# Kernel optimization log

Measured on AMD Instinct MI355X. Metric: run time of the kernel, lower is better.

The kernel has to match this reference:

```python
import jax, jax.numpy as jnp
import numpy as np

MAX_NODE = 20
SEG = [100, 20, 3200, 160, 400, 20, 400]  # split sizes, total 4300

_DIMS = {"h1": (5, 16), "h2": (16, 8), "h3": (8, 8),
         "f1": (8, 16), "f2": (16, 8), "f3": (8, 8),
         "d1": (13, 16), "d2": (16, 8), "d3": (8, 8),
         "g1": (8, 16), "g2": (16, 8), "g3": (8, 8),
         "fc1": (29, 32), "fc2": (32, 16), "fc3": (16, 8), "fc4": (8, 1)}


def _mk(key, shape):
    return jax.random.normal(key, shape, dtype=jnp.float32) * 0.1


def setup_inputs() -> dict:
    key = jax.random.key(0)
    ks = jax.random.split(key, 8 + 2 * len(_DIMS))
    # assemble the flat [1,4300] input: node feats, masks/adjacency summaries
    ni = jax.random.normal(ks[0], (100,), dtype=jnp.float32)
    valid = jax.random.bernoulli(ks[1], 0.8, (20,)).astype(jnp.float32)
    gmats = jax.random.uniform(ks[2], (3200,), dtype=jnp.float32)
    gmasks = jax.random.bernoulli(ks[3], 0.5, (160,)).astype(jnp.float32)
    summ = jax.random.bernoulli(ks[4], 0.3, (400,)).astype(jnp.float32)
    running = jax.random.bernoulli(ks[5], 0.5, (20,)).astype(jnp.float32)
    backmap = jax.random.bernoulli(ks[6], 0.3, (400,)).astype(jnp.float32)
    inp = jnp.concatenate([ni, valid, gmats, gmasks, summ, running, backmap])[None, :]
    out = {"input": inp}
    i = 8
    for name, (din, dout) in _DIMS.items():
        out[name + "_w"] = _mk(ks[i], (din, dout)); i += 1
        out[name + "_b"] = _mk(ks[i], (dout,)); i += 1
    return out


def reference(input, h1_w, h1_b, h2_w, h2_b, h3_w, h3_b,
              f1_w, f1_b, f2_w, f2_b, f3_w, f3_b,
              d1_w, d1_b, d2_w, d2_b, d3_w, d3_b,
              g1_w, g1_b, g2_w, g2_b, g3_w, g3_b,
              fc1_w, fc1_b, fc2_w, fc2_b, fc3_w, fc3_b, fc4_w, fc4_b):
    relu = jax.nn.relu
    gl = lambda x, w, b: x @ w + b
    x0 = input[0]
    ni = x0[:100].reshape(MAX_NODE, 5)
    valid = x0[100:120].reshape(1, 1, MAX_NODE)
    # x0[120:3320] = gcn_mats (split in original but never used)
    summ = x0[3480:3880].reshape(1, MAX_NODE, MAX_NODE)
    running = x0[3880:3900].reshape(1, 1, MAX_NODE)
    backmap = x0[3900:4300].reshape(1, MAX_NODE, MAX_NODE)
    # original overwrites every gcn_mask with zeros(20,1)
    zmask = jnp.zeros((MAX_NODE, 1), dtype=input.dtype)

    def fblock(y):
        for w, b in ((f1_w, f1_b), (f2_w, f2_b), (f3_w, f3_b),
                     (f1_w, f1_b), (f2_w, f2_b), (f3_w, f3_b)):
            y = relu(gl(y, w, b))
        return y

    x = relu(gl(ni, h1_w, h1_b))
    x = relu(gl(x, h2_w, h2_b))
    x = relu(gl(x, h3_w, h3_b))  # (20, 8)
    y = x
    for blk in range(8):
        src = y if blk == 5 else x  # block 5 forgets to reset y = x (as in source)
        y = fblock(src) * zmask
        x = x + y
    gcn_output = x  # (20, 8)

    xc = jnp.concatenate([ni, gcn_output], axis=1)  # (20, 13)
    s = relu(gl(xc, d1_w, d1_b))
    s = relu(gl(s, d2_w, d2_b))
    s = relu(gl(s, d3_w, d3_b))
    s = jnp.matmul(summ, s)  # (1, 20, 8)
    dag_summary = s
    s = relu(gl(s, g1_w, g1_b))
    s = relu(gl(s, g2_w, g2_b))
    s = relu(gl(s, g3_w, g3_b))
    global_summary = jnp.matmul(running, s)  # (1, 1, 8)
    dag_ext = jnp.matmul(backmap, dag_summary)  # (1, 20, 8)
    glob_ext = jnp.tile(global_summary, (1, MAX_NODE, 1))  # (1, 20, 8)

    merge = jnp.concatenate([ni[None], gcn_output[None], dag_ext, glob_ext], axis=2)  # (1,20,29)
    y2 = relu(gl(merge, fc1_w, fc1_b))
    y2 = relu(gl(y2, fc2_w, fc2_b))
    y2 = relu(gl(y2, fc3_w, fc3_b))
    logits = gl(y2, fc4_w, fc4_b).reshape(1, 1, MAX_NODE)
    logits = logits + (valid - 1.0) * 10000.0
    return jax.nn.softmax(logits, axis=-1).reshape(1, MAX_NODE)
```

## Files before the change

### kernel.cpp

```cpp
#include <hip/hip_runtime.h>
#include <math.h>

#define NT 64

#define CP4(dst, src, n) do { \
    const float4* _s4 = (const float4*)(src); float4* _d4 = (float4*)(dst); \
    for (int i = tid; i < (n) / 4; i += NT) _d4[i] = _s4[i]; } while (0)

template<int DIN, int DOUT, bool RELU>
__device__ __forceinline__ void dense20(int tid, const float* __restrict__ in,
                                        const float* __restrict__ w,
                                        const float* __restrict__ bi,
                                        float* __restrict__ out) {
    constexpr int N = 20 * DOUT;
    #pragma unroll
    for (int i0 = 0; i0 < N; i0 += NT) {
        int i = i0 + tid;
        if (i < N) {
            int r = i / DOUT, c = i % DOUT;
            float acc = bi[c];
            #pragma unroll
            for (int k = 0; k < DIN; ++k)
                acc = fmaf(in[r * DIN + k], w[k * DOUT + c], acc);
            out[i] = RELU ? fmaxf(acc, 0.0f) : acc;
        }
    }
}

__global__ __launch_bounds__(NT)
void fused_net_kernel(const float* __restrict__ inp,
                      const float* __restrict__ h1w, const float* __restrict__ h1b,
                      const float* __restrict__ h2w, const float* __restrict__ h2b,
                      const float* __restrict__ h3w, const float* __restrict__ h3b,
                      const float* __restrict__ d1w, const float* __restrict__ d1b,
                      const float* __restrict__ d2w, const float* __restrict__ d2b,
                      const float* __restrict__ d3w, const float* __restrict__ d3b,
                      const float* __restrict__ g1w, const float* __restrict__ g1b,
                      const float* __restrict__ g2w, const float* __restrict__ g2b,
                      const float* __restrict__ g3w, const float* __restrict__ g3b,
                      const float* __restrict__ fc1w, const float* __restrict__ fc1b,
                      const float* __restrict__ fc2w, const float* __restrict__ fc2b,
                      const float* __restrict__ fc3w, const float* __restrict__ fc3b,
                      const float* __restrict__ fc4w, const float* __restrict__ fc4b,
                      float* __restrict__ out) {
    const int tid = threadIdx.x;

    __shared__ __align__(16) float s_ni[100];
    __shared__ __align__(16) float s_valid[20];
    __shared__ __align__(16) float s_summ[400];
    __shared__ __align__(16) float s_run[20];
    __shared__ __align__(16) float s_back[400];
    __shared__ __align__(16) float s_h1w[80],  s_h1b[16];
    __shared__ __align__(16) float s_h2w[128], s_h2b[8];
    __shared__ __align__(16) float s_h3w[64],  s_h3b[8];
    __shared__ __align__(16) float s_d1w[208], s_d1b[16];
    __shared__ __align__(16) float s_d2w[128], s_d2b[8];
    __shared__ __align__(16) float s_d3w[64],  s_d3b[8];
    __shared__ __align__(16) float s_g1w[128], s_g1b[16];
    __shared__ __align__(16) float s_g2w[128], s_g2b[8];
    __shared__ __align__(16) float s_g3w[64],  s_g3b[8];
    __shared__ __align__(16) float s_fc1w[928], s_fc1b[32];
    __shared__ __align__(16) float s_fc2w[512], s_fc2b[16];
    __shared__ __align__(16) float s_fc3w[128], s_fc3b[8];
    __shared__ __align__(16) float s_fc4w[8];
    __shared__ float s_fc4b[1];
    __shared__ __align__(16) float s_bufA[640];
    __shared__ __align__(16) float s_bufB[640];
    __shared__ __align__(16) float s_gcn[160];
    __shared__ __align__(16) float s_dag[160];
    __shared__ __align__(16) float s_glob[8];
    __shared__ __align__(16) float s_logit[20];

    CP4(s_ni,    inp,        100);
    CP4(s_valid, inp + 100,  20);
    CP4(s_summ,  inp + 3480, 400);
    CP4(s_run,   inp + 3880, 20);
    CP4(s_back,  inp + 3900, 400);
    CP4(s_h1w, h1w, 80);   CP4(s_h1b, h1b, 16);
    CP4(s_h2w, h2w, 128);  CP4(s_h2b, h2b, 8);
    CP4(s_h3w, h3w, 64);   CP4(s_h3b, h3b, 8);
    CP4(s_d1w, d1w, 208);  CP4(s_d1b, d1b, 16);
    CP4(s_d2w, d2w, 128);  CP4(s_d2b, d2b, 8);
    CP4(s_d3w, d3w, 64);   CP4(s_d3b, d3b, 8);
    CP4(s_g1w, g1w, 128);  CP4(s_g1b, g1b, 16);
    CP4(s_g2w, g2w, 128);  CP4(s_g2b, g2b, 8);
    CP4(s_g3w, g3w, 64);   CP4(s_g3b, g3b, 8);
    CP4(s_fc1w, fc1w, 928); CP4(s_fc1b, fc1b, 32);
    CP4(s_fc2w, fc2w, 512); CP4(s_fc2b, fc2b, 16);
    CP4(s_fc3w, fc3w, 128); CP4(s_fc3b, fc3b, 8);
    CP4(s_fc4w, fc4w, 8);
    if (tid == 0) s_fc4b[0] = fc4b[0];
    __syncthreads();

    dense20<5, 16, true>(tid, s_ni,   s_h1w, s_h1b, s_bufA); __syncthreads();
    dense20<16, 8, true>(tid, s_bufA, s_h2w, s_h2b, s_bufB); __syncthreads();
    dense20<8,  8, true>(tid, s_bufB, s_h3w, s_h3b, s_gcn);  __syncthreads();

    #pragma unroll
    for (int i0 = 0; i0 < 320; i0 += NT) {
        int i = i0 + tid;
        int r = i >> 4, c = i & 15;
        float acc = s_d1b[c];
        #pragma unroll
        for (int k = 0; k < 5; ++k)
            acc = fmaf(s_ni[r * 5 + k], s_d1w[k * 16 + c], acc);
        #pragma unroll
        for (int k = 0; k < 8; ++k)
            acc = fmaf(s_gcn[r * 8 + k], s_d1w[(5 + k) * 16 + c], acc);
        s_bufA[i] = fmaxf(acc, 0.0f);
    }
    __syncthreads();
    dense20<16, 8, true>(tid, s_bufA, s_d2w, s_d2b, s_bufB); __syncthreads();
    dense20<8,  8, true>(tid, s_bufB, s_d3w, s_d3b, s_bufA); __syncthreads();

    #pragma unroll
    for (int i0 = 0; i0 < 192; i0 += NT) {
        int i = i0 + tid;
        if (i < 160) {
            int r = i >> 3, c = i & 7;
            float acc = 0.0f;
            #pragma unroll
            for (int k = 0; k < 20; ++k)
                acc = fmaf(s_summ[r * 20 + k], s_bufA[k * 8 + c], acc);
            s_dag[i] = acc;
        }
    }
    __syncthreads();

    dense20<8, 16, true>(tid, s_dag,  s_g1w, s_g1b, s_bufA); __syncthreads();
    dense20<16, 8, true>(tid, s_bufA, s_g2w, s_g2b, s_bufB); __syncthreads();
    dense20<8,  8, true>(tid, s_bufB, s_g3w, s_g3b, s_bufA); __syncthreads();

    #pragma unroll
    for (int i0 = 0; i0 < 192; i0 += NT) {
        int i = i0 + tid;
        if (i < 160) {
            int r = i >> 3, c = i & 7;
            float acc = 0.0f;
            #pragma unroll
            for (int k = 0; k < 20; ++k)
                acc = fmaf(s_back[r * 20 + k], s_dag[k * 8 + c], acc);
            s_bufB[i] = acc;
        } else if (i < 168) {
            int c = i - 160;
            float acc = 0.0f;
            #pragma unroll
            for (int k = 0; k < 20; ++k)
                acc = fmaf(s_run[k], s_bufA[k * 8 + c], acc);
            s_glob[c] = acc;
        }
    }
    __syncthreads();

    #pragma unroll
    for (int i0 = 0; i0 < 640; i0 += NT) {
        int i = i0 + tid;
        int r = i >> 5, c = i & 31;
        float acc = s_fc1b[c];
        #pragma unroll
        for (int k = 0; k < 5; ++k)
            acc = fmaf(s_ni[r * 5 + k], s_fc1w[k * 32 + c], acc);
        #pragma unroll
        for (int k = 0; k < 8; ++k)
            acc = fmaf(s_gcn[r * 8 + k], s_fc1w[(5 + k) * 32 + c], acc);
        #pragma unroll
        for (int k = 0; k < 8; ++k)
            acc = fmaf(s_bufB[r * 8 + k], s_fc1w[(13 + k) * 32 + c], acc);
        #pragma unroll
        for (int k = 0; k < 8; ++k)
            acc = fmaf(s_glob[k], s_fc1w[(21 + k) * 32 + c], acc);
        s_bufA[i] = fmaxf(acc, 0.0f);
    }
    __syncthreads();
    dense20<32, 16, true>(tid, s_bufA, s_fc2w, s_fc2b, s_bufB); __syncthreads();
    dense20<16, 8, true>(tid, s_bufB, s_fc3w, s_fc3b, s_dag);   __syncthreads();

    if (tid < 20) {
        float acc = s_fc4b[0];
        #pragma unroll
        for (int k = 0; k < 8; ++k)
            acc = fmaf(s_dag[tid * 8 + k], s_fc4w[k], acc);
        s_logit[tid] = acc + (s_valid[tid] - 1.0f) * 10000.0f;
    }
    __syncthreads();

    if (tid < 20) {
        float m = s_logit[0];
        #pragma unroll
        for (int r = 1; r < 20; ++r) m = fmaxf(m, s_logit[r]);
        float sum = 0.0f;
        #pragma unroll
        for (int r = 0; r < 20; ++r) sum += __expf(s_logit[r] - m);
        out[tid] = __expf(s_logit[tid] - m) / sum;
    }
}

extern "C" void kernel_launch(void* const* d_in, const int* in_sizes, int n_in,
                              void* d_out, int out_size, void* d_ws, size_t ws_size,
                              hipStream_t stream) {
    const float* inp = (const float*)d_in[0];
    const float* h1w = (const float*)d_in[1];  const float* h1b = (const float*)d_in[2];
    const float* h2w = (const float*)d_in[3];  const float* h2b = (const float*)d_in[4];
    const float* h3w = (const float*)d_in[5];  const float* h3b = (const float*)d_in[6];
    const float* d1w = (const float*)d_in[13]; const float* d1b = (const float*)d_in[14];
    const float* d2w = (const float*)d_in[15]; const float* d2b = (const float*)d_in[16];
    const float* d3w = (const float*)d_in[17]; const float* d3b = (const float*)d_in[18];
    const float* g1w = (const float*)d_in[19]; const float* g1b = (const float*)d_in[20];
    const float* g2w = (const float*)d_in[21]; const float* g2b = (const float*)d_in[22];
    const float* g3w = (const float*)d_in[23]; const float* g3b = (const float*)d_in[24];
    const float* fc1w = (const float*)d_in[25]; const float* fc1b = (const float*)d_in[26];
    const float* fc2w = (const float*)d_in[27]; const float* fc2b = (const float*)d_in[28];
    const float* fc3w = (const float*)d_in[29]; const float* fc3b = (const float*)d_in[30];
    const float* fc4w = (const float*)d_in[31]; const float* fc4b = (const float*)d_in[32];
    float* out = (float*)d_out;

    fused_net_kernel<<<1, NT, 0, stream>>>(inp,
        h1w, h1b, h2w, h2b, h3w, h3b,
        d1w, d1b, d2w, d2b, d3w, d3b,
        g1w, g1b, g2w, g2b, g3w, g3b,
        fc1w, fc1b, fc2w, fc2b, fc3w, fc3b, fc4w, fc4b,
        out);
}
```

Before: 130.1 us.

## Replace unrolled per-layer code with table-driven layer interpreter in shared arena

Rewrites the fused MLP kernel as a generic loop over a constant-memory layer descriptor table, with all weights and activations in one shared arena and concatenated inputs materialized explicitly. Block size grows from 64 to 256 threads and helper functions are noinline with unrolling disabled to shrink code size. The intent is to cut instruction footprint (icache misses) and spread work across more threads, at the cost of runtime-indexed loops, constant-memory descriptor loads and less compile-time specialization.

```diff
diff --git a/kernel.cpp b/kernel.cpp
--- a/kernel.cpp
+++ b/kernel.cpp
@@ -1,30 +1,87 @@
 #include <hip/hip_runtime.h>
 #include <math.h>
 
-#define NT 64
+#define NT 256
 
-#define CP4(dst, src, n) do { \
-    const float4* _s4 = (const float4*)(src); float4* _d4 = (float4*)(dst); \
-    for (int i = tid; i < (n) / 4; i += NT) _d4[i] = _s4[i]; } while (0)
+enum : int {
+  O_ZERO = 0,
+  O_NI   = 32,
+  O_VALID= 132,
+  O_SUMM = 152,
+  O_RUN  = 552,
+  O_BACK = 572,
+  O_H1W  = 972,    O_H1B = 1052,
+  O_H2W  = 1068,   O_H2B = 1196,
+  O_H3W  = 1204,   O_H3B = 1268,
+  O_D1W  = 1276,   O_D1B = 1484,
+  O_D2W  = 1500,   O_D2B = 1628,
+  O_D3W  = 1636,   O_D3B = 1700,
+  O_G1W  = 1708,   O_G1B = 1836,
+  O_G2W  = 1852,   O_G2B = 1980,
+  O_G3W  = 1988,   O_G3B = 2052,
+  O_FC1W = 2060,   O_FC1B = 2988,
+  O_FC2W = 3020,   O_FC2B = 3532,
+  O_FC3W = 3548,   O_FC3B = 3676,
+  O_FC4W = 3684,   O_FC4B = 3692,
+  O_B0   = 3696,
+  O_B1   = 4336,
+  O_GCN  = 4656,
+  O_CC1  = 4816,
+  O_CC2  = 5076,
+  O_DAG  = 5656,
+  O_DAGX = 5816,
+  O_GLOB = 5976,
+  O_LOGIT= 5984,
+  ARENA  = 6004
+};
 
-template<int DIN, int DOUT, bool RELU>
-__device__ __forceinline__ void dense20(int tid, const float* __restrict__ in,
-                                        const float* __restrict__ w,
-                                        const float* __restrict__ bi,
-                                        float* __restrict__ out) {
-    constexpr int N = 20 * DOUT;
-    #pragma unroll
-    for (int i0 = 0; i0 < N; i0 += NT) {
-        int i = i0 + tid;
-        if (i < N) {
-            int r = i / DOUT, c = i % DOUT;
-            float acc = bi[c];
-            #pragma unroll
-            for (int k = 0; k < DIN; ++k)
-                acc = fmaf(in[r * DIN + k], w[k * DOUT + c], acc);
-            out[i] = RELU ? fmaxf(acc, 0.0f) : acc;
-        }
+struct Ld { int rows, din, p, in, w, b, out, relu; };
+
+__constant__ Ld LT[16] = {
+  {20,  5, 4, O_NI,   O_H1W,  O_H1B,  O_B0,   1},
+  {20, 16, 3, O_B0,   O_H2W,  O_H2B,  O_B1,   1},
+  {20,  8, 3, O_B1,   O_H3W,  O_H3B,  O_GCN,  1},
+  {20, 13, 4, O_CC1,  O_D1W,  O_D1B,  O_B0,   1},
+  {20, 16, 3, O_B0,   O_D2W,  O_D2B,  O_B1,   1},
+  {20,  8, 3, O_B1,   O_D3W,  O_D3B,  O_B0,   1},
+  {20, 20, 3, O_SUMM, O_B0,   O_ZERO, O_DAG,  0},
+  {20,  8, 4, O_DAG,  O_G1W,  O_G1B,  O_B0,   1},
+  {20, 16, 3, O_B0,   O_G2W,  O_G2B,  O_B1,   1},
+  {20,  8, 3, O_B1,   O_G3W,  O_G3B,  O_B0,   1},
+  {20, 20, 3, O_BACK, O_DAG,  O_ZERO, O_DAGX, 0},
+  { 1, 20, 3, O_RUN,  O_B0,   O_ZERO, O_GLOB, 0},
+  {20, 29, 5, O_CC2,  O_FC1W, O_FC1B, O_B0,   1},
+  {20, 32, 4, O_B0,   O_FC2W, O_FC2B, O_B1,   1},
+  {20, 16, 3, O_B1,   O_FC3W, O_FC3B, O_B0,   1},
+  {20,  8, 0, O_B0,   O_FC4W, O_FC4B, O_LOGIT,0},
+};
+
+__device__ __attribute__((noinline))
+void run_layers(float* A, int lo, int hi, int tid) {
+  #pragma clang loop unroll(disable)
+  for (int L = lo; L < hi; ++L) {
+    Ld d = LT[L];
+    const int N = d.rows << d.p, msk = (1 << d.p) - 1, st = 1 << d.p;
+    #pragma clang loop unroll(disable)
+    for (int i = tid; i < N; i += NT) {
+      const int r = i >> d.p, c = i & msk;
+      float acc = A[d.b + c];
+      const float* in = A + d.in + r * d.din;
+      const float* wp = A + d.w + c;
+      #pragma unroll 4
+      for (int k = 0; k < d.din; ++k) { acc = fmaf(in[k], *wp, acc); wp += st; }
+      A[d.out + i] = d.relu ? fmaxf(acc, 0.0f) : acc;
     }
+    __syncthreads();
+  }
+}
+
+__device__ __attribute__((noinline))
+void cp4(float* A, int dst, const float* __restrict__ src, int n, int tid) {
+  float4* d4 = (float4*)(A + dst);
+  const float4* s4 = (const float4*)src;
+  #pragma clang loop unroll(disable)
+  for (int i = tid; i < (n >> 2); i += NT) d4[i] = s4[i];
 }
 
 __global__ __launch_bounds__(NT)
@@ -43,181 +100,99 @@
                       const float* __restrict__ fc3w, const float* __restrict__ fc3b,
                       const float* __restrict__ fc4w, const float* __restrict__ fc4b,
                       float* __restrict__ out) {
-    const int tid = threadIdx.x;
+  const int tid = threadIdx.x;
+  __shared__ __align__(16) float A[ARENA];
 
-    __shared__ __align__(16) float s_ni[100];
-    __shared__ __align__(16) float s_valid[20];
-    __shared__ __align__(16) float s_summ[400];
-    __shared__ __align__(16) float s_run[20];
-    __shared__ __align__(16) float s_back[400];
-    __shared__ __align__(16) float s_h1w[80],  s_h1b[16];
-    __shared__ __align__(16) float s_h2w[128], s_h2b[8];
-    __shared__ __align__(16) float s_h3w[64],  s_h3b[8];
-    __shared__ __align__(16) float s_d1w[208], s_d1b[16];
-    __shared__ __align__(16) float s_d2w[128], s_d2b[8];
-    __shared__ __align__(16) float s_d3w[64],  s_d3b[8];
-    __shared__ __align__(16) float s_g1w[128], s_g1b[16];
-    __shared__ __align__(16) float s_g2w[128], s_g2b[8];
-    __shared__ __align__(16) float s_g3w[64],  s_g3b[8];
-    __shared__ __align__(16) float s_fc1w[928], s_fc1b[32];
-    __shared__ __align__(16) float s_fc2w[512], s_fc2b[16];
-    __shared__ __align__(16) float s_fc3w[128], s_fc3b[8];
-    __shared__ __align__(16) float s_fc4w[8];
-    __shared__ float s_fc4b[1];
-    __shared__ __align__(16) float s_bufA[640];
-    __shared__ __align__(16) float s_bufB[640];
-    __shared__ __align__(16) float s_gcn[160];
-    __shared__ __align__(16) float s_dag[160];
-    __shared__ __align__(16) float s_glob[8];
-    __shared__ __align__(16) float s_logit[20];
+  if (tid < 32) A[O_ZERO + tid] = 0.0f;
+  cp4(A, O_NI,    inp,        100, tid);
+  cp4(A, O_VALID, inp + 100,  20,  tid);
+  cp4(A, O_SUMM,  inp + 3480, 400, tid);
+  cp4(A, O_RUN,   inp + 3880, 20,  tid);
+  cp4(A, O_BACK,  inp + 3900, 400, tid);
+  cp4(A, O_H1W, h1w, 80, tid);   cp4(A, O_H1B, h1b, 16, tid);
+  cp4(A, O_H2W, h2w, 128, tid);  cp4(A, O_H2B, h2b, 8, tid);
+  cp4(A, O_H3W, h3w, 64, tid);   cp4(A, O_H3B, h3b, 8, tid);
+  cp4(A, O_D1W, d1w, 208, tid);  cp4(A, O_D1B, d1b, 16, tid);
+  cp4(A, O_D2W, d2w, 128, tid);  cp4(A, O_D2B, d2b, 8, tid);
+  cp4(A, O_D3W, d3w, 64, tid);   cp4(A, O_D3B, d3b, 8, tid);
+  cp4(A, O_G1W, g1w, 128, tid);  cp4(A, O_G1B, g1b, 16, tid);
+  cp4(A, O_G2W, g2w, 128, tid);  cp4(A, O_G2B, g2b, 8, tid);
+  cp4(A, O_G3W, g3w, 64, tid);   cp4(A, O_G3B, g3b, 8, tid);
+  cp4(A, O_FC1W, fc1w, 928, tid); cp4(A, O_FC1B, fc1b, 32, tid);
+  cp4(A, O_FC2W, fc2w, 512, tid); cp4(A, O_FC2B, fc2b, 16, tid);
+  cp4(A, O_FC3W, fc3w, 128, tid); cp4(A, O_FC3B, fc3b, 8, tid);
+  cp4(A, O_FC4W, fc4w, 8, tid);
+  if (tid == 0) A[O_FC4B] = fc4b[0];
+  __syncthreads();
 
-    CP4(s_ni,    inp,        100);
-    CP4(s_valid, inp + 100,  20);
-    CP4(s_summ,  inp + 3480, 400);
-    CP4(s_run,   inp + 3880, 20);
-    CP4(s_back,  inp + 3900, 400);
-    CP4(s_h1w, h1w, 80);   CP4(s_h1b, h1b, 16);
-    CP4(s_h2w, h2w, 128);  CP4(s_h2b, h2b, 8);
-    CP4(s_h3w, h3w, 64);   CP4(s_h3b, h3b, 8);
-    CP4(s_d1w, d1w, 208);  CP4(s_d1b, d1b, 16);
-    CP4(s_d2w, d2w, 128);  CP4(s_d2b, d2b, 8);
-    CP4(s_d3w, d3w, 64);   CP4(s_d3b, d3b, 8);
-    CP4(s_g1w, g1w, 128);  CP4(s_g1b, g1b, 16);
-    CP4(s_g2w, g2w, 128);  CP4(s_g2b, g2b, 8);
-    CP4(s_g3w, g3w, 64);   CP4(s_g3b, g3b, 8);
-    CP4(s_fc1w, fc1w, 928); CP4(s_fc1b, fc1b, 32);
-    CP4(s_fc2w, fc2w, 512); CP4(s_fc2b, fc2b, 16);
-    CP4(s_fc3w, fc3w, 128); CP4(s_fc3b, fc3b, 8);
-    CP4(s_fc4w, fc4w, 8);
-    if (tid == 0) s_fc4b[0] = fc4b[0];
-    __syncthreads();
+  #pragma clang loop unroll(disable)
+  for (int i = tid; i < 100; i += NT) {
+    int r = i / 5, c = i - r * 5;
+    float v = A[O_NI + i];
+    A[O_CC1 + r * 13 + c] = v;
+    A[O_CC2 + r * 29 + c] = v;
+  }
 
-    dense20<5, 16, true>(tid, s_ni,   s_h1w, s_h1b, s_bufA); __syncthreads();
-    dense20<16, 8, true>(tid, s_bufA, s_h2w, s_h2b, s_bufB); __syncthreads();
-    dense20<8,  8, true>(tid, s_bufB, s_h3w, s_h3b, s_gcn);  __syncthreads();
+  run_layers(A, 0, 3, tid);
 
-    #pragma unroll
-    for (int i0 = 0; i0 < 320; i0 += NT) {
-        int i = i0 + tid;
-        int r = i >> 4, c = i & 15;
-        float acc = s_d1b[c];
-        #pragma unroll
-        for (int k = 0; k < 5; ++k)
-            acc = fmaf(s_ni[r * 5 + k], s_d1w[k * 16 + c], acc);
-        #pragma unroll
-        for (int k = 0; k < 8; ++k)
-            acc = fmaf(s_gcn[r * 8 + k], s_d1w[(5 + k) * 16 + c], acc);
-        s_bufA[i] = fmaxf(acc, 0.0f);
-    }
-    __syncthreads();
-    dense20<16, 8, true>(tid, s_bufA, s_d2w, s_d2b, s_bufB); __syncthreads();
-    dense20<8,  8, true>(tid, s_bufB, s_d3w, s_d3b, s_bufA); __syncthreads();
+  #pragma clang loop unroll(disable)
+  for (int i = tid; i < 160; i += NT) {
+    int r = i >> 3, c = i & 7;
+    float v = A[O_GCN + i];
+    A[O_CC1 + r * 13 + 5 + c] = v;
+    A[O_CC2 + r * 29 + 5 + c] = v;
+  }
+  __syncthreads();
 
-    #pragma unroll
-    for (int i0 = 0; i0 < 192; i0 += NT) {
-        int i = i0 + tid;
-        if (i < 160) {
-            int r = i >> 3, c = i & 7;
-            float acc = 0.0f;
-            #pragma unroll
-            for (int k = 0; k < 20; ++k)
-                acc = fmaf(s_summ[r * 20 + k], s_bufA[k * 8 + c], acc);
-            s_dag[i] = acc;
-        }
-    }
-    __syncthreads();
+  run_layers(A, 3, 12, tid);
 
-    dense20<8, 16, true>(tid, s_dag,  s_g1w, s_g1b, s_bufA); __syncthreads();
-    dense20<16, 8, true>(tid, s_bufA, s_g2w, s_g2b, s_bufB); __syncthreads();
-    dense20<8,  8, true>(tid, s_bufB, s_g3w, s_g3b, s_bufA); __syncthreads();
+  #pragma clang loop unroll(disable)
+  for (int i = tid; i < 160; i += NT) {
+    int r = i >> 3, c = i & 7;
+    A[O_CC2 + r * 29 + 13 + c] = A[O_DAGX + i];
+    A[O_CC2 + r * 29 + 21 + c] = A[O_GLOB + c];
+  }
+  __syncthreads();
 
-    #pragma unroll
-    for (int i0 = 0; i0 < 192; i0 += NT) {
-        int i = i0 + tid;
-        if (i < 160) {
-            int r = i >> 3, c = i & 7;
-            float acc = 0.0f;
-            #pragma unroll
-            for (int k = 0; k < 20; ++k)
-                acc = fmaf(s_back[r * 20 + k], s_dag[k * 8 + c], acc);
-            s_bufB[i] = acc;
-        } else if (i < 168) {
-            int c = i - 160;
-            float acc = 0.0f;
-            #pragma unroll
-            for (int k = 0; k < 20; ++k)
-                acc = fmaf(s_run[k], s_bufA[k * 8 + c], acc);
-            s_glob[c] = acc;
-        }
-    }
-    __syncthreads();
+  run_layers(A, 12, 16, tid);
 
-    #pragma unroll
-    for (int i0 = 0; i0 < 640; i0 += NT) {
-        int i = i0 + tid;
-        int r = i >> 5, c = i & 31;
-        float acc = s_fc1b[c];
-        #pragma unroll
-        for (int k = 0; k < 5; ++k)
-            acc = fmaf(s_ni[r * 5 + k], s_fc1w[k * 32 + c], acc);
-        #pragma unroll
-        for (int k = 0; k < 8; ++k)
-            acc = fmaf(s_gcn[r * 8 + k], s_fc1w[(5 + k) * 32 + c], acc);
-        #pragma unroll
-        for (int k = 0; k < 8; ++k)
-            acc = fmaf(s_bufB[r * 8 + k], s_fc1w[(13 + k) * 32 + c], acc);
-        #pragma unroll
-        for (int k = 0; k < 8; ++k)
-            acc = fmaf(s_glob[k], s_fc1w[(21 + k) * 32 + c], acc);
-        s_bufA[i] = fmaxf(acc, 0.0f);
-    }
-    __syncthreads();
-    dense20<32, 16, true>(tid, s_bufA, s_fc2w, s_fc2b, s_bufB); __syncthreads();
-    dense20<16, 8, true>(tid, s_bufB, s_fc3w, s_fc3b, s_dag);   __syncthreads();
-
-    if (tid < 20) {
-        float acc = s_fc4b[0];
-        #pragma unroll
-        for (int k = 0; k < 8; ++k)
-            acc = fmaf(s_dag[tid * 8 + k], s_fc4w[k], acc);
-        s_logit[tid] = acc + (s_valid[tid] - 1.0f) * 10000.0f;
-    }
-    __syncthreads();
-
-    if (tid < 20) {
-        float m = s_logit[0];
-        #pragma unroll
-        for (int r = 1; r < 20; ++r) m = fmaxf(m, s_logit[r]);
-        float sum = 0.0f;
-        #pragma unroll
-        for (int r = 0; r < 20; ++r) sum += __expf(s_logit[r] - m);
-        out[tid] = __expf(s_logit[tid] - m) / sum;
-    }
+  if (tid < 20)
+    A[O_LOGIT + tid] += (A[O_VALID + tid] - 1.0f) * 10000.0f;
+  __syncthreads();
+  if (tid < 20) {
+    float m = A[O_LOGIT + 0];
+    #pragma clang loop unroll(disable)
+    for (int r = 1; r < 20; ++r) m = fmaxf(m, A[O_LOGIT + r]);
+    float sum = 0.0f;
+    #pragma clang loop unroll(disable)
+    for (int r = 0; r < 20; ++r) sum += __expf(A[O_LOGIT + r] - m);
+    out[tid] = __expf(A[O_LOGIT + tid] - m) / sum;
+  }
 }
 
 extern "C" void kernel_launch(void* const* d_in, const int* in_sizes, int n_in,
                               void* d_out, int out_size, void* d_ws, size_t ws_size,
                               hipStream_t stream) {
-    const float* inp = (const float*)d_in[0];
-    const float* h1w = (const float*)d_in[1];  const float* h1b = (const float*)d_in[2];
-    const float* h2w = (const float*)d_in[3];  const float* h2b = (const float*)d_in[4];
-    const float* h3w = (const float*)d_in[5];  const float* h3b = (const float*)d_in[6];
-    const float* d1w = (const float*)d_in[13]; const float* d1b = (const float*)d_in[14];
-    const float* d2w = (const float*)d_in[15]; const float* d2b = (const float*)d_in[16];
-    const float* d3w = (const float*)d_in[17]; const float* d3b = (const float*)d_in[18];
-    const float* g1w = (const float*)d_in[19]; const float* g1b = (const float*)d_in[20];
-    const float* g2w = (const float*)d_in[21]; const float* g2b = (const float*)d_in[22];
-    const float* g3w = (const float*)d_in[23]; const float* g3b = (const float*)d_in[24];
-    const float* fc1w = (const float*)d_in[25]; const float* fc1b = (const float*)d_in[26];
-    const float* fc2w = (const float*)d_in[27]; const float* fc2b = (const float*)d_in[28];
-    const float* fc3w = (const float*)d_in[29]; const float* fc3b = (const float*)d_in[30];
-    const float* fc4w = (const float*)d_in[31]; const float* fc4b = (const float*)d_in[32];
-    float* out = (float*)d_out;
+  const float* inp = (const float*)d_in[0];
+  const float* h1w = (const float*)d_in[1];  const float* h1b = (const float*)d_in[2];
+  const float* h2w = (const float*)d_in[3];  const float* h2b = (const float*)d_in[4];
+  const float* h3w = (const float*)d_in[5];  const float* h3b = (const float*)d_in[6];
+  const float* d1w = (const float*)d_in[13]; const float* d1b = (const float*)d_in[14];
+  const float* d2w = (const float*)d_in[15]; const float* d2b = (const float*)d_in[16];
+  const float* d3w = (const float*)d_in[17]; const float* d3b = (const float*)d_in[18];
+  const float* g1w = (const float*)d_in[19]; const float* g1b = (const float*)d_in[20];
+  const float* g2w = (const float*)d_in[21]; const float* g2b = (const float*)d_in[22];
+  const float* g3w = (const float*)d_in[23]; const float* g3b = (const float*)d_in[24];
+  const float* fc1w = (const float*)d_in[25]; const float* fc1b = (const float*)d_in[26];
+  const float* fc2w = (const float*)d_in[27]; const float* fc2b = (const float*)d_in[28];
+  const float* fc3w = (const float*)d_in[29]; const float* fc3b = (const float*)d_in[30];
+  const float* fc4w = (const float*)d_in[31]; const float* fc4b = (const float*)d_in[32];
+  float* out = (float*)d_out;
 
-    fused_net_kernel<<<1, NT, 0, stream>>>(inp,
-        h1w, h1b, h2w, h2b, h3w, h3b,
-        d1w, d1b, d2w, d2b, d3w, d3b,
-        g1w, g1b, g2w, g2b, g3w, g3b,
-        fc1w, fc1b, fc2w, fc2b, fc3w, fc3b, fc4w, fc4b,
-        out);
+  fused_net_kernel<<<1, NT, 0, stream>>>(inp,
+      h1w, h1b, h2w, h2b, h3w, h3b,
+      d1w, d1b, d2w, d2b, d3w, d3b,
+      g1w, g1b, g2w, g2b, g3w, g3b,
+      fc1w, fc1b, fc2w, fc2b, fc3w, fc3b, fc4w, fc4b,
+      out);
 }
```

Result: slower. 135.9 us (+4.5%).
